# Kernel tuning notes

Measured on AMD Instinct MI355X. Metric: run time of the kernel, lower is better.

Reference implementation:

```python
import jax, jax.numpy as jnp
import numpy as np

BN_EPS = 1e-5

@jax.custom_vjp
def ste_sign(x):
    return jnp.sign(x)

def _ste_fwd(x):
    return jnp.sign(x), x

def _ste_bwd(x, g):
    # straight-through estimator with hardtanh clipping
    return (g * (jnp.abs(x) <= 1.0).astype(g.dtype),)

ste_sign.defvjp(_ste_fwd, _ste_bwd)

def bi_conv_bn_relu(h, W, scale, gamma, beta):
    # h: [B, Cin, K, N]; W: [Cout, Cin] (1x1 conv); scale/gamma/beta: [Cout]
    ba = ste_sign(h)                      # binarize activations
    bw = ste_sign(W)                      # binarize weights
    y = jnp.einsum('oi,bikn->bokn', bw, ba) * scale[None, :, None, None]
    # BatchNorm2d, training-mode batch statistics over (B, K, N)
    mean = jnp.mean(y, axis=(0, 2, 3), keepdims=True)
    var = jnp.var(y, axis=(0, 2, 3), keepdims=True)
    y = gamma[None, :, None, None] * (y - mean) * jax.lax.rsqrt(var + BN_EPS) + beta[None, :, None, None]
    return jax.nn.relu(y)

def setup_inputs() -> dict:
    key = jax.random.key(0)
    sizes = [64, 64, 64, 128]
    B, N, K = 8, 1024, 32
    ks = jax.random.split(key, 16)
    inp = {"agg_feat": jax.random.normal(ks[0], (B * N, K, sizes[0]), dtype=jnp.float32)}
    j = 1
    for i in range(1, len(sizes)):
        cin, cout = sizes[i - 1], sizes[i]
        inp[f"W{i}"] = jax.random.normal(ks[j], (cout, cin), dtype=jnp.float32) * 0.1; j += 1
        inp[f"s{i}"] = jax.random.uniform(ks[j], (cout,), dtype=jnp.float32, minval=0.05, maxval=0.2); j += 1
        inp[f"g{i}"] = jnp.ones((cout,), dtype=jnp.float32)
        inp[f"b{i}"] = jnp.zeros((cout,), dtype=jnp.float32)
    return inp

def reference(agg_feat, W1, s1, g1, b1, W2, s2, g2, b2, W3, s3, g3, b3):
    B = 8
    M, K, D = agg_feat.shape
    # view(B, -1, K, D).permute(0, 3, 2, 1) -> [B, D, K, N]
    h = agg_feat.reshape(B, M // B, K, D).transpose(0, 3, 2, 1)
    h = bi_conv_bn_relu(h, W1, s1, g1, b1)
    h = bi_conv_bn_relu(h, W2, s2, g2, b2)
    h = bi_conv_bn_relu(h, W3, s3, g3, b3)
    h = jnp.max(h, axis=2)                 # max-pool over neighbors -> [B, C, N]
    C = h.shape[1]
    return h.transpose(0, 2, 1).reshape(-1, C)  # [B*N, C]
```

## Files before the change

### kernel.cpp

```cpp
#include <hip/hip_runtime.h>


typedef unsigned long long u64;
typedef unsigned int u32;

#define P_TOTAL (8192 * 32)
#define NREP 16

__device__ __forceinline__ u64 bcast64(u64 x, int p) {
    unsigned lo = __builtin_amdgcn_readlane((unsigned)x, p);
    unsigned hi = __builtin_amdgcn_readlane((unsigned)(x >> 32), p);
    return ((u64)hi << 32) | lo;
}

__device__ __forceinline__ u64 pack_stats(int sd, int sq) {
    return ((u64)(unsigned)sd << 32) | (u64)(unsigned)sq;
}

__device__ __forceinline__ void affine_from_stats(const u64* __restrict__ st,
        int c, const float* __restrict__ scale, const float* __restrict__ gamma,
        const float* __restrict__ beta, int cparam, float& a, float& b) {
    u64 v = 0;
    #pragma unroll
    for (int r = 0; r < NREP; ++r) v += st[r * 256 + c];
    int sd = (int)(v >> 32);
    int sq = (int)(unsigned)(v & 0xFFFFFFFFull);
    const double invN = 1.0 / (double)P_TOTAL;
    double m = (double)sd * invN;
    double var = (double)sq * invN - m * m;
    double sc = (double)scale[cparam];
    double inv = 1.0 / sqrt(sc * sc * var + 1e-5);
    double g = (double)gamma[cparam];
    a = (float)(g * inv * sc);
    b = (float)((double)beta[cparam] - g * inv * sc * m);
}

__device__ __forceinline__ int make_thresh(float a, float b, bool& flip) {
    if (a == 0.f) { flip = false; return (b > 0.f) ? -65 : 65; }
    double r = -(double)b / (double)a;
    r = fmin(fmax(r, -1e6), 1e6);
    int t0 = (int)floor(r);
    int T;
    if (a > 0.f) {
        flip = false;
        T = t0 + 2;
        if (fmaf(a, (float)(t0 + 1), b) > 0.f) T = t0 + 1;
        if (fmaf(a, (float)(t0    ), b) > 0.f) T = t0;
        if (fmaf(a, (float)(t0 - 1), b) > 0.f) T = t0 - 1;
    } else {
        flip = true;
        int H = t0 - 2;
        if (fmaf(a, (float)(t0 - 1), b) > 0.f) H = t0 - 1;
        if (fmaf(a, (float)(t0    ), b) > 0.f) H = t0;
        if (fmaf(a, (float)(t0 + 1), b) > 0.f) H = t0 + 1;
        T = -H;
    }
    return max(-65, min(65, T));
}

__device__ __forceinline__ void block_params(const u64* __restrict__ stats,
        int stat_off, const float* __restrict__ scale, const float* __restrict__ gamma,
        const float* __restrict__ beta, int* gT, int* gF) {
    const int t = threadIdx.x;
    if (t < 64) {
        float a, b;
        affine_from_stats(stats, stat_off + t, scale, gamma, beta, t, a, b);
        bool flip;
        gT[t] = make_thresh(a, b, flip);
        gF[t] = flip ? 1 : 0;
    }
    __syncthreads();
}

__global__ void __launch_bounds__(256) k0_pack(
    const float* __restrict__ W1, const float* __restrict__ W2,
    const float* __restrict__ W3, ulonglong2* __restrict__ wp1,
    ulonglong2* __restrict__ wp2, ulonglong2* __restrict__ wp3,
    u64* __restrict__ stats) {
    const int t = threadIdx.x;
    #pragma unroll
    for (int r = 0; r < NREP; ++r) stats[r * 256 + t] = 0;

    const float* src;
    ulonglong2* dst;
    bool perm, l1;
    if (t < 64)       { src = W1 + t * 64;         dst = wp1 + t;         perm = true;  l1 = true;  }
    else if (t < 128) { src = W2 + (t - 64) * 64;  dst = wp2 + (t - 64);  perm = false; l1 = false; }
    else              { src = W3 + (t - 128) * 64; dst = wp3 + (t - 128); perm = false; l1 = false; }

    const float4* s4 = (const float4*)src;
    float4 v[16];
    #pragma unroll
    for (int j = 0; j < 16; ++j) v[j] = s4[j];

    u64 hiM = 0, loM = 0;
    #pragma unroll
    for (int j = 0; j < 16; ++j) {
        const float e0 = v[j].x, e1 = v[j].y, e2 = v[j].z, e3 = v[j].w;
        #pragma unroll
        for (int k = 0; k < 4; ++k) {
            const float w = (k == 0) ? e0 : (k == 1) ? e1 : (k == 2) ? e2 : e3;
            const int c = 4 * j + k;
            const int p = perm ? (((c & 3) << 4) | (c >> 2)) : c;
            const bool bh = (w > 0.f);
            const bool bl = l1 ? (w != 0.f) : (w < 0.f);
            if (bh) hiM |= 1ull << p;
            if (bl) loM |= 1ull << p;
        }
    }
    *dst = make_ulonglong2(hiM, loM);
}

__global__ void __launch_bounds__(256) k1_pack_stats(
    const float4* __restrict__ in4, const ulonglong2* __restrict__ wp1,
    ulonglong2* __restrict__ A1, u64* __restrict__ stats) {
    const int lane = threadIdx.x & 63;
    const int wib = threadIdx.x >> 6;
    const int wid = (blockIdx.x << 2) | wib;
    const ulonglong2 w = wp1[lane];
    const int sh = (lane >> 4) << 4;
    const size_t base = (size_t)wid * 512 + lane;

    float4 v0 = in4[base];
    float4 v1 = in4[base + 64];
    float4 v2 = in4[base + 128];
    float4 v3 = in4[base + 192];
    float4 v4 = in4[base + 256];
    float4 v5 = in4[base + 320];
    float4 v6 = in4[base + 384];
    float4 v7 = in4[base + 448];

    int sd = 0, sq = 0;
    auto proc = [&](float4 v, int q0) {
        u64 bs0 = __ballot(v.x > 0.f), bn0 = __ballot(v.x != 0.f);
        u64 bs1 = __ballot(v.y > 0.f), bn1 = __ballot(v.y != 0.f);
        u64 bs2 = __ballot(v.z > 0.f), bn2 = __ballot(v.z != 0.f);
        u64 bs3 = __ballot(v.w > 0.f), bn3 = __ballot(v.w != 0.f);
        u64 myS = ((bs0 >> sh) & 0xFFFFull) | (((bs1 >> sh) & 0xFFFFull) << 16)
                | (((bs2 >> sh) & 0xFFFFull) << 32) | (((bs3 >> sh) & 0xFFFFull) << 48);
        u64 myN = ((bn0 >> sh) & 0xFFFFull) | (((bn1 >> sh) & 0xFFFFull) << 16)
                | (((bn2 >> sh) & 0xFFFFull) << 32) | (((bn3 >> sh) & 0xFFFFull) << 48);
        if ((lane & 15) == 0) A1[q0 + (lane >> 4)] = make_ulonglong2(myS, myN);
        #pragma unroll
        for (int p = 0; p < 4; ++p) {
            const int s2 = p << 4;
            u64 as = ((bs0 >> s2) & 0xFFFFull) | (((bs1 >> s2) & 0xFFFFull) << 16)
                   | (((bs2 >> s2) & 0xFFFFull) << 32) | (((bs3 >> s2) & 0xFFFFull) << 48);
            u64 an = ((bn0 >> s2) & 0xFFFFull) | (((bn1 >> s2) & 0xFFFFull) << 16)
                   | (((bn2 >> s2) & 0xFFFFull) << 32) | (((bn3 >> s2) & 0xFFFFull) << 48);
            u64 mnz = an & w.y;
            int dot = __popcll(mnz) - 2 * __popcll(mnz & (as ^ w.x));
            sd += dot; sq += dot * dot;
        }
    };
    const int q_base = wid * 32;
    proc(v0, q_base);      proc(v1, q_base + 4);
    proc(v2, q_base + 8);  proc(v3, q_base + 12);
    proc(v4, q_base + 16); proc(v5, q_base + 20);
    proc(v6, q_base + 24); proc(v7, q_base + 28);

    __shared__ int rd[4][64], rq[4][64];
    rd[wib][lane] = sd; rq[wib][lane] = sq;
    __syncthreads();
    if (threadIdx.x < 64) {
        int td = rd[0][lane] + rd[1][lane] + rd[2][lane] + rd[3][lane];
        int tq = rq[0][lane] + rq[1][lane] + rq[2][lane] + rq[3][lane];
        atomicAdd(&stats[(blockIdx.x & (NREP - 1)) * 256 + lane], pack_stats(td, tq));
    }
}

__global__ void __launch_bounds__(256) k2_bin1_stats2(
    const ulonglong2* __restrict__ A1, const ulonglong2* __restrict__ wp1,
    const ulonglong2* __restrict__ wp2, const float* __restrict__ scale,
    const float* __restrict__ gamma, const float* __restrict__ beta,
    u64* __restrict__ A2, u64* __restrict__ stats) {
    __shared__ int gT[64], gF[64];
    block_params(stats, 0, scale, gamma, beta, gT, gF);

    const int lane = threadIdx.x & 63;
    const int wib = threadIdx.x >> 6;
    const int wid = (blockIdx.x << 2) | wib;
    const int T = gT[lane];
    const bool flip = gF[lane] != 0;
    ulonglong2 w1 = wp1[lane];
    const u64 w1S = flip ? ~w1.x : w1.x;
    const u64 w1N = w1.y;
    const ulonglong2 w2 = wp2[lane];

    const u64 av = ((const u64*)A1)[(size_t)wid * 64 + lane];
    u64 mymask = 0;
    int sd = 0, sq = 0;
    #pragma unroll 8
    for (int p = 0; p < 32; ++p) {
        u64 as = bcast64(av, 2 * p);
        u64 an = bcast64(av, 2 * p + 1);
        u64 mnz = an & w1N;
        int dot1 = __popcll(mnz) - 2 * __popcll(mnz & (as ^ w1S));
        u64 A = __ballot(dot1 >= T);
        if (lane == p) mymask = A;
        int d2 = __popcll(A & w2.x) - __popcll(A & w2.y);
        sd += d2; sq += d2 * d2;
    }
    if (lane < 32) A2[(size_t)wid * 32 + lane] = mymask;

    __shared__ int rd[4][64], rq[4][64];
    rd[wib][lane] = sd; rq[wib][lane] = sq;
    __syncthreads();
    if (threadIdx.x < 64) {
        int td = rd[0][lane] + rd[1][lane] + rd[2][lane] + rd[3][lane];
        int tq = rq[0][lane] + rq[1][lane] + rq[2][lane] + rq[3][lane];
        atomicAdd(&stats[(blockIdx.x & (NREP - 1)) * 256 + 64 + lane], pack_stats(td, tq));
    }
}

__global__ void __launch_bounds__(256) k3_bin2_stats3(
    const u64* __restrict__ A2, const ulonglong2* __restrict__ wp2,
    const ulonglong2* __restrict__ wp3, const float* __restrict__ scale,
    const float* __restrict__ gamma, const float* __restrict__ beta,
    short* __restrict__ dmm, u64* __restrict__ stats) {
    __shared__ int gT[64], gF[64];
    block_params(stats, 64, scale, gamma, beta, gT, gF);

    const int lane = threadIdx.x & 63;
    const int wib = threadIdx.x >> 6;
    const int wid = (blockIdx.x << 2) | wib;
    const int T = gT[lane];
    const bool flip = gF[lane] != 0;
    const ulonglong2 w2 = wp2[lane];
    const u64 w2P = flip ? w2.y : w2.x;
    const u64 w2N = flip ? w2.x : w2.y;
    const ulonglong2 w3a = wp3[lane];
    const ulonglong2 w3b = wp3[lane + 64];

    const u32 a32 = ((const u32*)A2)[(size_t)wid * 64 + lane];
    int sda = 0, sqa = 0, sdb = 0, sqb = 0;
    int maxa = -127, mina = 127, maxb = -127, minb = 127;
    #pragma unroll 8
    for (int p = 0; p < 32; ++p) {
        u32 lo = __builtin_amdgcn_readlane(a32, 2 * p);
        u32 hi = __builtin_amdgcn_readlane(a32, 2 * p + 1);
        u64 A = ((u64)hi << 32) | lo;
        int d2 = __popcll(A & w2P) - __popcll(A & w2N);
        u64 A3 = __ballot(d2 >= T);
        int da = __popcll(A3 & w3a.x) - __popcll(A3 & w3a.y);
        int db = __popcll(A3 & w3b.x) - __popcll(A3 & w3b.y);
        sda += da; sqa += da * da; sdb += db; sqb += db * db;
        maxa = max(maxa, da); mina = min(mina, da);
        maxb = max(maxb, db); minb = min(minb, db);
    }
    dmm[wid * 128 + lane]      = (short)((maxa & 0xFF) | ((mina & 0xFF) << 8));
    dmm[wid * 128 + 64 + lane] = (short)((maxb & 0xFF) | ((minb & 0xFF) << 8));

    __shared__ int rda[4][64], rqa[4][64], rdb[4][64], rqb[4][64];
    rda[wib][lane] = sda; rqa[wib][lane] = sqa;
    rdb[wib][lane] = sdb; rqb[wib][lane] = sqb;
    __syncthreads();
    if (threadIdx.x < 64) {
        const int rep = (blockIdx.x & (NREP - 1)) * 256;
        int tda = rda[0][lane] + rda[1][lane] + rda[2][lane] + rda[3][lane];
        int tqa = rqa[0][lane] + rqa[1][lane] + rqa[2][lane] + rqa[3][lane];
        int tdb = rdb[0][lane] + rdb[1][lane] + rdb[2][lane] + rdb[3][lane];
        int tqb = rqb[0][lane] + rqb[1][lane] + rqb[2][lane] + rqb[3][lane];
        atomicAdd(&stats[rep + 128 + lane], pack_stats(tda, tqa));
        atomicAdd(&stats[rep + 192 + lane], pack_stats(tdb, tqb));
    }
}

__global__ void __launch_bounds__(512) k4_out(
    const short* __restrict__ dmm, const float* __restrict__ scale,
    const float* __restrict__ gamma, const float* __restrict__ beta,
    const u64* __restrict__ stats, float* __restrict__ out) {
    __shared__ float sa[128], sb[128];
    if (threadIdx.x < 128)
        affine_from_stats(stats, 128 + threadIdx.x, scale, gamma, beta,
                          threadIdx.x, sa[threadIdx.x], sb[threadIdx.x]);
    __syncthreads();
    const int idx = blockIdx.x * 512 + threadIdx.x;
    const int o = idx & 127;
    short pk = dmm[idx];
    int mx = (signed char)(pk & 0xFF);
    int mn = (signed char)((pk >> 8) & 0xFF);
    float a = sa[o], b = sb[o];
    float v = fmaf(a, (float)(a >= 0.f ? mx : mn), b);
    out[idx] = fmaxf(v, 0.f);
}

extern "C" void kernel_launch(void* const* d_in, const int* in_sizes, int n_in,
                              void* d_out, int out_size, void* d_ws, size_t ws_size,
                              hipStream_t stream) {
    const float* agg = (const float*)d_in[0];
    const float* W1 = (const float*)d_in[1];
    const float* s1 = (const float*)d_in[2];
    const float* g1 = (const float*)d_in[3];
    const float* b1 = (const float*)d_in[4];
    const float* W2 = (const float*)d_in[5];
    const float* s2 = (const float*)d_in[6];
    const float* g2 = (const float*)d_in[7];
    const float* b2 = (const float*)d_in[8];
    const float* W3 = (const float*)d_in[9];
    const float* s3 = (const float*)d_in[10];
    const float* g3 = (const float*)d_in[11];
    const float* b3 = (const float*)d_in[12];
    float* out = (float*)d_out;

    char* ws = (char*)d_ws;
    ulonglong2* wp1 = (ulonglong2*)(ws + 0);
    ulonglong2* wp2 = (ulonglong2*)(ws + 1024);
    ulonglong2* wp3 = (ulonglong2*)(ws + 2048);
    u64* stats = (u64*)(ws + 4096);
    ulonglong2* A1 = (ulonglong2*)(ws + 65536);
    u64* A2 = (u64*)(ws + 65536 + (size_t)P_TOTAL * 16);
    short* dmm = (short*)(ws + 65536 + (size_t)P_TOTAL * 24);

    k0_pack<<<1, 256, 0, stream>>>(W1, W2, W3, wp1, wp2, wp3, stats);
    k1_pack_stats<<<2048, 256, 0, stream>>>((const float4*)agg, wp1, A1, stats);
    k2_bin1_stats2<<<2048, 256, 0, stream>>>(A1, wp1, wp2, s1, g1, b1, A2, stats);
    k3_bin2_stats3<<<2048, 256, 0, stream>>>(A2, wp2, wp3, s2, g2, b2, dmm, stats);
    k4_out<<<2048, 512, 0, stream>>>(dmm, s3, g3, b3, stats, out);
}
```

Before: 72.18 us.

## Fuse all stages into one persistent kernel with grid-wide barriers

Replaces the five-kernel pipeline with a stats-zeroing kernel and a single persistent kernel of 512 blocks. Each wave keeps its binarized intermediate masks in registers across the three layers and synchronizes via atomic grid barriers between the batch-norm statistics phases. This removes the global-memory round trips for the A1/A2/dmm intermediates and the extra kernel launches. In exchange it relies on all 512 blocks being co-resident (launch bounds 256,2) and adds spin-wait barrier latency.

```diff
diff --git a/kernel.cpp b/kernel.cpp
--- a/kernel.cpp
+++ b/kernel.cpp
@@ -6,6 +6,7 @@
 
 #define P_TOTAL (8192 * 32)
 #define NREP 16
+#define NBLK 512
 
 __device__ __forceinline__ u64 bcast64(u64 x, int p) {
     unsigned lo = __builtin_amdgcn_readlane((unsigned)x, p);
@@ -17,12 +18,17 @@
     return ((u64)(unsigned)sd << 32) | (u64)(unsigned)sq;
 }
 
-__device__ __forceinline__ void affine_from_stats(const u64* __restrict__ st,
-        int c, const float* __restrict__ scale, const float* __restrict__ gamma,
+__device__ __forceinline__ void stat_add(u64* p, u64 v) {
+    __hip_atomic_fetch_add(p, v, __ATOMIC_RELEASE, __HIP_MEMORY_SCOPE_AGENT);
+}
+
+__device__ __forceinline__ void affine_from_stats(u64* st, int c,
+        const float* __restrict__ scale, const float* __restrict__ gamma,
         const float* __restrict__ beta, int cparam, float& a, float& b) {
     u64 v = 0;
     #pragma unroll
-    for (int r = 0; r < NREP; ++r) v += st[r * 256 + c];
+    for (int r = 0; r < NREP; ++r)
+        v += __hip_atomic_load(&st[r * 256 + c], __ATOMIC_RELAXED, __HIP_MEMORY_SCOPE_AGENT);
     int sd = (int)(v >> 32);
     int sq = (int)(unsigned)(v & 0xFFFFFFFFull);
     const double invN = 1.0 / (double)P_TOTAL;
@@ -58,237 +64,226 @@
     return max(-65, min(65, T));
 }
 
-__device__ __forceinline__ void block_params(const u64* __restrict__ stats,
-        int stat_off, const float* __restrict__ scale, const float* __restrict__ gamma,
-        const float* __restrict__ beta, int* gT, int* gF) {
-    const int t = threadIdx.x;
-    if (t < 64) {
-        float a, b;
-        affine_from_stats(stats, stat_off + t, scale, gamma, beta, t, a, b);
-        bool flip;
-        gT[t] = make_thresh(a, b, flip);
-        gF[t] = flip ? 1 : 0;
-    }
-    __syncthreads();
-}
-
-__global__ void __launch_bounds__(256) k0_pack(
-    const float* __restrict__ W1, const float* __restrict__ W2,
-    const float* __restrict__ W3, ulonglong2* __restrict__ wp1,
-    ulonglong2* __restrict__ wp2, ulonglong2* __restrict__ wp3,
-    u64* __restrict__ stats) {
-    const int t = threadIdx.x;
-    #pragma unroll
-    for (int r = 0; r < NREP; ++r) stats[r * 256 + t] = 0;
-
-    const float* src;
-    ulonglong2* dst;
-    bool perm, l1;
-    if (t < 64)       { src = W1 + t * 64;         dst = wp1 + t;         perm = true;  l1 = true;  }
-    else if (t < 128) { src = W2 + (t - 64) * 64;  dst = wp2 + (t - 64);  perm = false; l1 = false; }
-    else              { src = W3 + (t - 128) * 64; dst = wp3 + (t - 128); perm = false; l1 = false; }
-
-    const float4* s4 = (const float4*)src;
-    float4 v[16];
-    #pragma unroll
-    for (int j = 0; j < 16; ++j) v[j] = s4[j];
-
-    u64 hiM = 0, loM = 0;
-    #pragma unroll
-    for (int j = 0; j < 16; ++j) {
-        const float e0 = v[j].x, e1 = v[j].y, e2 = v[j].z, e3 = v[j].w;
-        #pragma unroll
-        for (int k = 0; k < 4; ++k) {
-            const float w = (k == 0) ? e0 : (k == 1) ? e1 : (k == 2) ? e2 : e3;
-            const int c = 4 * j + k;
-            const int p = perm ? (((c & 3) << 4) | (c >> 2)) : c;
-            const bool bh = (w > 0.f);
-            const bool bl = l1 ? (w != 0.f) : (w < 0.f);
-            if (bh) hiM |= 1ull << p;
-            if (bl) loM |= 1ull << p;
-        }
-    }
-    *dst = make_ulonglong2(hiM, loM);
-}
-
-__global__ void __launch_bounds__(256) k1_pack_stats(
-    const float4* __restrict__ in4, const ulonglong2* __restrict__ wp1,
-    ulonglong2* __restrict__ A1, u64* __restrict__ stats) {
+__device__ __forceinline__ void gbar(u32* bar, int k) {
+    __syncthreads();
+    if (threadIdx.x == 0) {
+        __hip_atomic_fetch_add(&bar[k], 1u, __ATOMIC_ACQ_REL, __HIP_MEMORY_SCOPE_AGENT);
+        while (__hip_atomic_load(&bar[k], __ATOMIC_ACQUIRE, __HIP_MEMORY_SCOPE_AGENT) < (u32)NBLK)
+            __builtin_amdgcn_s_sleep(2);
+    }
+    __syncthreads();
+}
+
+__global__ void k_zero(u64* __restrict__ stats, u32* __restrict__ bar) {
+    stats[blockIdx.x * 256 + threadIdx.x] = 0;
+    if (blockIdx.x == 0 && threadIdx.x < 16) bar[threadIdx.x] = 0;
+}
+
+__global__ void __launch_bounds__(256, 2) kmain(
+    const float4* __restrict__ in4,
+    const float* __restrict__ W1, const float* __restrict__ s1,
+    const float* __restrict__ g1, const float* __restrict__ b1,
+    const float* __restrict__ W2, const float* __restrict__ s2,
+    const float* __restrict__ g2, const float* __restrict__ b2,
+    const float* __restrict__ W3, const float* __restrict__ s3,
+    const float* __restrict__ g3, const float* __restrict__ b3,
+    float* __restrict__ out, u64* __restrict__ stats, u32* __restrict__ bar) {
     const int lane = threadIdx.x & 63;
     const int wib = threadIdx.x >> 6;
-    const int wid = (blockIdx.x << 2) | wib;
-    const ulonglong2 w = wp1[lane];
-    const int sh = (lane >> 4) << 4;
-    const size_t base = (size_t)wid * 512 + lane;
-
-    float4 v0 = in4[base];
-    float4 v1 = in4[base + 64];
-    float4 v2 = in4[base + 128];
-    float4 v3 = in4[base + 192];
-    float4 v4 = in4[base + 256];
-    float4 v5 = in4[base + 320];
-    float4 v6 = in4[base + 384];
-    float4 v7 = in4[base + 448];
-
-    int sd = 0, sq = 0;
-    auto proc = [&](float4 v, int q0) {
-        u64 bs0 = __ballot(v.x > 0.f), bn0 = __ballot(v.x != 0.f);
-        u64 bs1 = __ballot(v.y > 0.f), bn1 = __ballot(v.y != 0.f);
-        u64 bs2 = __ballot(v.z > 0.f), bn2 = __ballot(v.z != 0.f);
-        u64 bs3 = __ballot(v.w > 0.f), bn3 = __ballot(v.w != 0.f);
-        u64 myS = ((bs0 >> sh) & 0xFFFFull) | (((bs1 >> sh) & 0xFFFFull) << 16)
-                | (((bs2 >> sh) & 0xFFFFull) << 32) | (((bs3 >> sh) & 0xFFFFull) << 48);
-        u64 myN = ((bn0 >> sh) & 0xFFFFull) | (((bn1 >> sh) & 0xFFFFull) << 16)
-                | (((bn2 >> sh) & 0xFFFFull) << 32) | (((bn3 >> sh) & 0xFFFFull) << 48);
-        if ((lane & 15) == 0) A1[q0 + (lane >> 4)] = make_ulonglong2(myS, myN);
-        #pragma unroll
-        for (int p = 0; p < 4; ++p) {
-            const int s2 = p << 4;
-            u64 as = ((bs0 >> s2) & 0xFFFFull) | (((bs1 >> s2) & 0xFFFFull) << 16)
-                   | (((bs2 >> s2) & 0xFFFFull) << 32) | (((bs3 >> s2) & 0xFFFFull) << 48);
-            u64 an = ((bn0 >> s2) & 0xFFFFull) | (((bn1 >> s2) & 0xFFFFull) << 16)
-                   | (((bn2 >> s2) & 0xFFFFull) << 32) | (((bn3 >> s2) & 0xFFFFull) << 48);
-            u64 mnz = an & w.y;
-            int dot = __popcll(mnz) - 2 * __popcll(mnz & (as ^ w.x));
-            sd += dot; sq += dot * dot;
-        }
-    };
-    const int q_base = wid * 32;
-    proc(v0, q_base);      proc(v1, q_base + 4);
-    proc(v2, q_base + 8);  proc(v3, q_base + 12);
-    proc(v4, q_base + 16); proc(v5, q_base + 20);
-    proc(v6, q_base + 24); proc(v7, q_base + 28);
-
-    __shared__ int rd[4][64], rq[4][64];
-    rd[wib][lane] = sd; rq[wib][lane] = sq;
-    __syncthreads();
+    const int gw = blockIdx.x * 4 + wib;
+    const int rep = (blockIdx.x & (NREP - 1)) * 256;
+
+    __shared__ int rda[4][64], rqa[4][64], rdb[4][64], rqb[4][64];
+    __shared__ int gT[64], gF[64];
+    __shared__ float sA[128], sB[128];
+
+    u64 w1S = 0, w1N = 0, w2P = 0, w2N = 0, w3aP = 0, w3aN = 0, w3bP = 0, w3bN = 0;
+    {
+        const float4* r1 = (const float4*)(W1 + lane * 64);
+        const float4* r2 = (const float4*)(W2 + lane * 64);
+        const float4* r3a = (const float4*)(W3 + lane * 64);
+        const float4* r3b = (const float4*)(W3 + (lane + 64) * 64);
+        #pragma unroll
+        for (int j = 0; j < 16; ++j) {
+            float4 a = r1[j], b = r2[j], c = r3a[j], d = r3b[j];
+            #pragma unroll
+            for (int k = 0; k < 4; ++k) {
+                const int ch = 4 * j + k;
+                const int p1 = ((ch & 3) << 4) | (ch >> 2);
+                float wa = (k == 0) ? a.x : (k == 1) ? a.y : (k == 2) ? a.z : a.w;
+                float wb = (k == 0) ? b.x : (k == 1) ? b.y : (k == 2) ? b.z : b.w;
+                float wc = (k == 0) ? c.x : (k == 1) ? c.y : (k == 2) ? c.z : c.w;
+                float wd = (k == 0) ? d.x : (k == 1) ? d.y : (k == 2) ? d.z : d.w;
+                if (wa > 0.f)  w1S |= 1ull << p1;
+                if (wa != 0.f) w1N |= 1ull << p1;
+                if (wb > 0.f)  w2P |= 1ull << ch;
+                if (wb < 0.f)  w2N |= 1ull << ch;
+                if (wc > 0.f)  w3aP |= 1ull << ch;
+                if (wc < 0.f)  w3aN |= 1ull << ch;
+                if (wd > 0.f)  w3bP |= 1ull << ch;
+                if (wd < 0.f)  w3bN |= 1ull << ch;
+            }
+        }
+    }
+
+    u64 a1s[4], a1n[4];
+    {
+        int sd = 0, sq = 0;
+        #pragma unroll
+        for (int un = 0; un < 4; ++un) {
+            const size_t base = (size_t)(4 * gw + un) * 512 + lane;
+            float4 v0 = in4[base];
+            float4 v1 = in4[base + 64];
+            float4 v2 = in4[base + 128];
+            float4 v3 = in4[base + 192];
+            float4 v4 = in4[base + 256];
+            float4 v5 = in4[base + 320];
+            float4 v6 = in4[base + 384];
+            float4 v7 = in4[base + 448];
+            u64 ms = 0, mn = 0;
+            auto proc = [&](float4 v, int b) {
+                u64 bs0 = __ballot(v.x > 0.f), bn0 = __ballot(v.x != 0.f);
+                u64 bs1 = __ballot(v.y > 0.f), bn1 = __ballot(v.y != 0.f);
+                u64 bs2 = __ballot(v.z > 0.f), bn2 = __ballot(v.z != 0.f);
+                u64 bs3 = __ballot(v.w > 0.f), bn3 = __ballot(v.w != 0.f);
+                #pragma unroll
+                for (int p = 0; p < 4; ++p) {
+                    const int s2 = p << 4;
+                    u64 as = ((bs0 >> s2) & 0xFFFFull) | (((bs1 >> s2) & 0xFFFFull) << 16)
+                           | (((bs2 >> s2) & 0xFFFFull) << 32) | (((bs3 >> s2) & 0xFFFFull) << 48);
+                    u64 an = ((bn0 >> s2) & 0xFFFFull) | (((bn1 >> s2) & 0xFFFFull) << 16)
+                           | (((bn2 >> s2) & 0xFFFFull) << 32) | (((bn3 >> s2) & 0xFFFFull) << 48);
+                    u64 mnz = an & w1N;
+                    int dot = __popcll(mnz) - 2 * __popcll(mnz & (as ^ w1S));
+                    sd += dot; sq += dot * dot;
+                    if (lane == b * 4 + p) { ms = as; mn = an; }
+                }
+            };
+            proc(v0, 0); proc(v1, 1); proc(v2, 2); proc(v3, 3);
+            proc(v4, 4); proc(v5, 5); proc(v6, 6); proc(v7, 7);
+            a1s[un] = ms; a1n[un] = mn;
+        }
+        rda[wib][lane] = sd; rqa[wib][lane] = sq;
+        __syncthreads();
+        if (threadIdx.x < 64) {
+            int td = rda[0][lane] + rda[1][lane] + rda[2][lane] + rda[3][lane];
+            int tq = rqa[0][lane] + rqa[1][lane] + rqa[2][lane] + rqa[3][lane];
+            stat_add(&stats[rep + lane], pack_stats(td, tq));
+            __threadfence();
+        }
+    }
+    gbar(bar, 0);
+
     if (threadIdx.x < 64) {
-        int td = rd[0][lane] + rd[1][lane] + rd[2][lane] + rd[3][lane];
-        int tq = rq[0][lane] + rq[1][lane] + rq[2][lane] + rq[3][lane];
-        atomicAdd(&stats[(blockIdx.x & (NREP - 1)) * 256 + lane], pack_stats(td, tq));
-    }
-}
-
-__global__ void __launch_bounds__(256) k2_bin1_stats2(
-    const ulonglong2* __restrict__ A1, const ulonglong2* __restrict__ wp1,
-    const ulonglong2* __restrict__ wp2, const float* __restrict__ scale,
-    const float* __restrict__ gamma, const float* __restrict__ beta,
-    u64* __restrict__ A2, u64* __restrict__ stats) {
-    __shared__ int gT[64], gF[64];
-    block_params(stats, 0, scale, gamma, beta, gT, gF);
-
-    const int lane = threadIdx.x & 63;
-    const int wib = threadIdx.x >> 6;
-    const int wid = (blockIdx.x << 2) | wib;
-    const int T = gT[lane];
-    const bool flip = gF[lane] != 0;
-    ulonglong2 w1 = wp1[lane];
-    const u64 w1S = flip ? ~w1.x : w1.x;
-    const u64 w1N = w1.y;
-    const ulonglong2 w2 = wp2[lane];
-
-    const u64 av = ((const u64*)A1)[(size_t)wid * 64 + lane];
-    u64 mymask = 0;
-    int sd = 0, sq = 0;
-    #pragma unroll 8
-    for (int p = 0; p < 32; ++p) {
-        u64 as = bcast64(av, 2 * p);
-        u64 an = bcast64(av, 2 * p + 1);
-        u64 mnz = an & w1N;
-        int dot1 = __popcll(mnz) - 2 * __popcll(mnz & (as ^ w1S));
-        u64 A = __ballot(dot1 >= T);
-        if (lane == p) mymask = A;
-        int d2 = __popcll(A & w2.x) - __popcll(A & w2.y);
-        sd += d2; sq += d2 * d2;
-    }
-    if (lane < 32) A2[(size_t)wid * 32 + lane] = mymask;
-
-    __shared__ int rd[4][64], rq[4][64];
-    rd[wib][lane] = sd; rq[wib][lane] = sq;
-    __syncthreads();
+        float a, b;
+        affine_from_stats(stats, threadIdx.x, s1, g1, b1, threadIdx.x, a, b);
+        bool fl;
+        gT[threadIdx.x] = make_thresh(a, b, fl);
+        gF[threadIdx.x] = fl ? 1 : 0;
+    }
+    __syncthreads();
+    u64 a2m[4];
+    {
+        const int T = gT[lane];
+        const u64 w1Sf = gF[lane] ? ~w1S : w1S;
+        int sd = 0, sq = 0;
+        #pragma unroll
+        for (int un = 0; un < 4; ++un) {
+            u64 mymask = 0;
+            #pragma unroll 8
+            for (int p = 0; p < 32; ++p) {
+                u64 as = bcast64(a1s[un], p);
+                u64 an = bcast64(a1n[un], p);
+                u64 mnz = an & w1N;
+                int dot1 = __popcll(mnz) - 2 * __popcll(mnz & (as ^ w1Sf));
+                u64 A = __ballot(dot1 >= T);
+                if (lane == p) mymask = A;
+                int d2 = __popcll(A & w2P) - __popcll(A & w2N);
+                sd += d2; sq += d2 * d2;
+            }
+            a2m[un] = mymask;
+        }
+        __syncthreads();
+        rda[wib][lane] = sd; rqa[wib][lane] = sq;
+        __syncthreads();
+        if (threadIdx.x < 64) {
+            int td = rda[0][lane] + rda[1][lane] + rda[2][lane] + rda[3][lane];
+            int tq = rqa[0][lane] + rqa[1][lane] + rqa[2][lane] + rqa[3][lane];
+            stat_add(&stats[rep + 64 + lane], pack_stats(td, tq));
+            __threadfence();
+        }
+    }
+    gbar(bar, 1);
+
     if (threadIdx.x < 64) {
-        int td = rd[0][lane] + rd[1][lane] + rd[2][lane] + rd[3][lane];
-        int tq = rq[0][lane] + rq[1][lane] + rq[2][lane] + rq[3][lane];
-        atomicAdd(&stats[(blockIdx.x & (NREP - 1)) * 256 + 64 + lane], pack_stats(td, tq));
-    }
-}
-
-__global__ void __launch_bounds__(256) k3_bin2_stats3(
-    const u64* __restrict__ A2, const ulonglong2* __restrict__ wp2,
-    const ulonglong2* __restrict__ wp3, const float* __restrict__ scale,
-    const float* __restrict__ gamma, const float* __restrict__ beta,
-    short* __restrict__ dmm, u64* __restrict__ stats) {
-    __shared__ int gT[64], gF[64];
-    block_params(stats, 64, scale, gamma, beta, gT, gF);
-
-    const int lane = threadIdx.x & 63;
-    const int wib = threadIdx.x >> 6;
-    const int wid = (blockIdx.x << 2) | wib;
-    const int T = gT[lane];
-    const bool flip = gF[lane] != 0;
-    const ulonglong2 w2 = wp2[lane];
-    const u64 w2P = flip ? w2.y : w2.x;
-    const u64 w2N = flip ? w2.x : w2.y;
-    const ulonglong2 w3a = wp3[lane];
-    const ulonglong2 w3b = wp3[lane + 64];
-
-    const u32 a32 = ((const u32*)A2)[(size_t)wid * 64 + lane];
-    int sda = 0, sqa = 0, sdb = 0, sqb = 0;
-    int maxa = -127, mina = 127, maxb = -127, minb = 127;
-    #pragma unroll 8
-    for (int p = 0; p < 32; ++p) {
-        u32 lo = __builtin_amdgcn_readlane(a32, 2 * p);
-        u32 hi = __builtin_amdgcn_readlane(a32, 2 * p + 1);
-        u64 A = ((u64)hi << 32) | lo;
-        int d2 = __popcll(A & w2P) - __popcll(A & w2N);
-        u64 A3 = __ballot(d2 >= T);
-        int da = __popcll(A3 & w3a.x) - __popcll(A3 & w3a.y);
-        int db = __popcll(A3 & w3b.x) - __popcll(A3 & w3b.y);
-        sda += da; sqa += da * da; sdb += db; sqb += db * db;
-        maxa = max(maxa, da); mina = min(mina, da);
-        maxb = max(maxb, db); minb = min(minb, db);
-    }
-    dmm[wid * 128 + lane]      = (short)((maxa & 0xFF) | ((mina & 0xFF) << 8));
-    dmm[wid * 128 + 64 + lane] = (short)((maxb & 0xFF) | ((minb & 0xFF) << 8));
-
-    __shared__ int rda[4][64], rqa[4][64], rdb[4][64], rqb[4][64];
-    rda[wib][lane] = sda; rqa[wib][lane] = sqa;
-    rdb[wib][lane] = sdb; rqb[wib][lane] = sqb;
-    __syncthreads();
-    if (threadIdx.x < 64) {
-        const int rep = (blockIdx.x & (NREP - 1)) * 256;
-        int tda = rda[0][lane] + rda[1][lane] + rda[2][lane] + rda[3][lane];
-        int tqa = rqa[0][lane] + rqa[1][lane] + rqa[2][lane] + rqa[3][lane];
-        int tdb = rdb[0][lane] + rdb[1][lane] + rdb[2][lane] + rdb[3][lane];
-        int tqb = rqb[0][lane] + rqb[1][lane] + rqb[2][lane] + rqb[3][lane];
-        atomicAdd(&stats[rep + 128 + lane], pack_stats(tda, tqa));
-        atomicAdd(&stats[rep + 192 + lane], pack_stats(tdb, tqb));
-    }
-}
-
-__global__ void __launch_bounds__(512) k4_out(
-    const short* __restrict__ dmm, const float* __restrict__ scale,
-    const float* __restrict__ gamma, const float* __restrict__ beta,
-    const u64* __restrict__ stats, float* __restrict__ out) {
-    __shared__ float sa[128], sb[128];
-    if (threadIdx.x < 128)
-        affine_from_stats(stats, 128 + threadIdx.x, scale, gamma, beta,
-                          threadIdx.x, sa[threadIdx.x], sb[threadIdx.x]);
-    __syncthreads();
-    const int idx = blockIdx.x * 512 + threadIdx.x;
-    const int o = idx & 127;
-    short pk = dmm[idx];
-    int mx = (signed char)(pk & 0xFF);
-    int mn = (signed char)((pk >> 8) & 0xFF);
-    float a = sa[o], b = sb[o];
-    float v = fmaf(a, (float)(a >= 0.f ? mx : mn), b);
-    out[idx] = fmaxf(v, 0.f);
+        float a, b;
+        affine_from_stats(stats, 64 + threadIdx.x, s2, g2, b2, threadIdx.x, a, b);
+        bool fl;
+        gT[threadIdx.x] = make_thresh(a, b, fl);
+        gF[threadIdx.x] = fl ? 1 : 0;
+    }
+    __syncthreads();
+    int mxa[4], mna[4], mxb[4], mnb[4];
+    {
+        const int T = gT[lane];
+        const u64 w2Pf = gF[lane] ? w2N : w2P;
+        const u64 w2Nf = gF[lane] ? w2P : w2N;
+        int sda = 0, sqa = 0, sdb = 0, sqb = 0;
+        #pragma unroll
+        for (int un = 0; un < 4; ++un) {
+            int xa = -127, na = 127, xb = -127, nb = 127;
+            #pragma unroll 8
+            for (int p = 0; p < 32; ++p) {
+                u64 A = bcast64(a2m[un], p);
+                int d2 = __popcll(A & w2Pf) - __popcll(A & w2Nf);
+                u64 A3 = __ballot(d2 >= T);
+                int da = __popcll(A3 & w3aP) - __popcll(A3 & w3aN);
+                int db = __popcll(A3 & w3bP) - __popcll(A3 & w3bN);
+                sda += da; sqa += da * da; sdb += db; sqb += db * db;
+                xa = max(xa, da); na = min(na, da);
+                xb = max(xb, db); nb = min(nb, db);
+            }
+            mxa[un] = xa; mna[un] = na; mxb[un] = xb; mnb[un] = nb;
+        }
+        __syncthreads();
+        rda[wib][lane] = sda; rqa[wib][lane] = sqa;
+        rdb[wib][lane] = sdb; rqb[wib][lane] = sqb;
+        __syncthreads();
+        if (threadIdx.x < 64) {
+            int tda = rda[0][lane] + rda[1][lane] + rda[2][lane] + rda[3][lane];
+            int tqa = rqa[0][lane] + rqa[1][lane] + rqa[2][lane] + rqa[3][lane];
+            int tdb = rdb[0][lane] + rdb[1][lane] + rdb[2][lane] + rdb[3][lane];
+            int tqb = rqb[0][lane] + rqb[1][lane] + rqb[2][lane] + rqb[3][lane];
+            stat_add(&stats[rep + 128 + lane], pack_stats(tda, tqa));
+            stat_add(&stats[rep + 192 + lane], pack_stats(tdb, tqb));
+            __threadfence();
+        }
+    }
+    gbar(bar, 2);
+
+    if (threadIdx.x < 128) {
+        affine_from_stats(stats, 128 + threadIdx.x, s3, g3, b3, threadIdx.x,
+                          sA[threadIdx.x], sB[threadIdx.x]);
+    }
+    __syncthreads();
+    {
+        const float aa = sA[lane], ba = sB[lane];
+        const float ab = sA[64 + lane], bb = sB[64 + lane];
+        #pragma unroll
+        for (int un = 0; un < 4; ++un) {
+            const int m = 4 * gw + un;
+            float va = fmaf(aa, (float)(aa >= 0.f ? mxa[un] : mna[un]), ba);
+            float vb = fmaf(ab, (float)(ab >= 0.f ? mxb[un] : mnb[un]), bb);
+            out[(size_t)m * 128 + lane] = fmaxf(va, 0.f);
+            out[(size_t)m * 128 + 64 + lane] = fmaxf(vb, 0.f);
+        }
+    }
 }
 
 extern "C" void kernel_launch(void* const* d_in, const int* in_sizes, int n_in,
                               void* d_out, int out_size, void* d_ws, size_t ws_size,
                               hipStream_t stream) {
-    const float* agg = (const float*)d_in[0];
+    const float4* in4 = (const float4*)d_in[0];
     const float* W1 = (const float*)d_in[1];
     const float* s1 = (const float*)d_in[2];
     const float* g1 = (const float*)d_in[3];
@@ -302,19 +297,10 @@
     const float* g3 = (const float*)d_in[11];
     const float* b3 = (const float*)d_in[12];
     float* out = (float*)d_out;
-
-    char* ws = (char*)d_ws;
-    ulonglong2* wp1 = (ulonglong2*)(ws + 0);
-    ulonglong2* wp2 = (ulonglong2*)(ws + 1024);
-    ulonglong2* wp3 = (ulonglong2*)(ws + 2048);
-    u64* stats = (u64*)(ws + 4096);
-    ulonglong2* A1 = (ulonglong2*)(ws + 65536);
-    u64* A2 = (u64*)(ws + 65536 + (size_t)P_TOTAL * 16);
-    short* dmm = (short*)(ws + 65536 + (size_t)P_TOTAL * 24);
-
-    k0_pack<<<1, 256, 0, stream>>>(W1, W2, W3, wp1, wp2, wp3, stats);
-    k1_pack_stats<<<2048, 256, 0, stream>>>((const float4*)agg, wp1, A1, stats);
-    k2_bin1_stats2<<<2048, 256, 0, stream>>>(A1, wp1, wp2, s1, g1, b1, A2, stats);
-    k3_bin2_stats3<<<2048, 256, 0, stream>>>(A2, wp2, wp3, s2, g2, b2, dmm, stats);
-    k4_out<<<2048, 512, 0, stream>>>(dmm, s3, g3, b3, stats, out);
-}
+    u64* stats = (u64*)d_ws;
+    u32* bar = (u32*)((char*)d_ws + 32768);
+
+    k_zero<<<16, 256, 0, stream>>>(stats, bar);
+    kmain<<<NBLK, 256, 0, stream>>>(in4, W1, s1, g1, b1, W2, s2, g2, b2,
+                                    W3, s3, g3, b3, out, stats, bar);
+}
```

New measurement: 220.8 us. 3.06x slower.

## Fold weight packing into each kernel and replace pack kernel with memset

Applied to the files above, without the earlier changes.

Removes the single-block weight-packing kernel. Each consumer kernel now packs the binarized weight rows it needs into shared memory, and the stats buffer is cleared with an async memset. The BN threshold computation runs in parallel with the weight packing on separate thread groups. The inner loops of k2 and k3 are fully unrolled with two independent accumulator sets to shorten the dependency chains. In exchange, every block repeats the weight loads and packing, which adds redundant global reads and prologue latency per block.

```diff
diff --git a/kernel.cpp b/kernel.cpp
--- a/kernel.cpp
+++ b/kernel.cpp
@@ -58,66 +58,42 @@
     return max(-65, min(65, T));
 }
 
-__device__ __forceinline__ void block_params(const u64* __restrict__ stats,
-        int stat_off, const float* __restrict__ scale, const float* __restrict__ gamma,
-        const float* __restrict__ beta, int* gT, int* gF) {
-    const int t = threadIdx.x;
-    if (t < 64) {
-        float a, b;
-        affine_from_stats(stats, stat_off + t, scale, gamma, beta, t, a, b);
-        bool flip;
-        gT[t] = make_thresh(a, b, flip);
-        gF[t] = flip ? 1 : 0;
-    }
-    __syncthreads();
-}
-
-__global__ void __launch_bounds__(256) k0_pack(
-    const float* __restrict__ W1, const float* __restrict__ W2,
-    const float* __restrict__ W3, ulonglong2* __restrict__ wp1,
-    ulonglong2* __restrict__ wp2, ulonglong2* __restrict__ wp3,
-    u64* __restrict__ stats) {
-    const int t = threadIdx.x;
-    #pragma unroll
-    for (int r = 0; r < NREP; ++r) stats[r * 256 + t] = 0;
-
-    const float* src;
-    ulonglong2* dst;
-    bool perm, l1;
-    if (t < 64)       { src = W1 + t * 64;         dst = wp1 + t;         perm = true;  l1 = true;  }
-    else if (t < 128) { src = W2 + (t - 64) * 64;  dst = wp2 + (t - 64);  perm = false; l1 = false; }
-    else              { src = W3 + (t - 128) * 64; dst = wp3 + (t - 128); perm = false; l1 = false; }
-
+__device__ __forceinline__ void pack_row(const float* __restrict__ src, bool perm,
+                                         bool l1m, u64& hiM, u64& loM) {
     const float4* s4 = (const float4*)src;
-    float4 v[16];
-    #pragma unroll
-    for (int j = 0; j < 16; ++j) v[j] = s4[j];
-
-    u64 hiM = 0, loM = 0;
+    hiM = 0; loM = 0;
     #pragma unroll
     for (int j = 0; j < 16; ++j) {
-        const float e0 = v[j].x, e1 = v[j].y, e2 = v[j].z, e3 = v[j].w;
+        float4 v = s4[j];
         #pragma unroll
         for (int k = 0; k < 4; ++k) {
-            const float w = (k == 0) ? e0 : (k == 1) ? e1 : (k == 2) ? e2 : e3;
+            const float w = (k == 0) ? v.x : (k == 1) ? v.y : (k == 2) ? v.z : v.w;
             const int c = 4 * j + k;
             const int p = perm ? (((c & 3) << 4) | (c >> 2)) : c;
             const bool bh = (w > 0.f);
-            const bool bl = l1 ? (w != 0.f) : (w < 0.f);
+            const bool bl = l1m ? (w != 0.f) : (w < 0.f);
             if (bh) hiM |= 1ull << p;
             if (bl) loM |= 1ull << p;
         }
     }
-    *dst = make_ulonglong2(hiM, loM);
 }
 
 __global__ void __launch_bounds__(256) k1_pack_stats(
-    const float4* __restrict__ in4, const ulonglong2* __restrict__ wp1,
+    const float4* __restrict__ in4, const float* __restrict__ W1,
     ulonglong2* __restrict__ A1, u64* __restrict__ stats) {
+    __shared__ u64 wl[128];
+    if (threadIdx.x < 64) {
+        u64 h, l;
+        pack_row(W1 + threadIdx.x * 64, true, true, h, l);
+        wl[2 * threadIdx.x] = h;
+        wl[2 * threadIdx.x + 1] = l;
+    }
+    __syncthreads();
+
     const int lane = threadIdx.x & 63;
     const int wib = threadIdx.x >> 6;
     const int wid = (blockIdx.x << 2) | wib;
-    const ulonglong2 w = wp1[lane];
+    const u64 w1S = wl[2 * lane], w1N = wl[2 * lane + 1];
     const int sh = (lane >> 4) << 4;
     const size_t base = (size_t)wid * 512 + lane;
 
@@ -148,8 +124,8 @@
                    | (((bs2 >> s2) & 0xFFFFull) << 32) | (((bs3 >> s2) & 0xFFFFull) << 48);
             u64 an = ((bn0 >> s2) & 0xFFFFull) | (((bn1 >> s2) & 0xFFFFull) << 16)
                    | (((bn2 >> s2) & 0xFFFFull) << 32) | (((bn3 >> s2) & 0xFFFFull) << 48);
-            u64 mnz = an & w.y;
-            int dot = __popcll(mnz) - 2 * __popcll(mnz & (as ^ w.x));
+            u64 mnz = an & w1N;
+            int dot = __popcll(mnz) - 2 * __popcll(mnz & (as ^ w1S));
             sd += dot; sq += dot * dot;
         }
     };
@@ -170,41 +146,73 @@
 }
 
 __global__ void __launch_bounds__(256) k2_bin1_stats2(
-    const ulonglong2* __restrict__ A1, const ulonglong2* __restrict__ wp1,
-    const ulonglong2* __restrict__ wp2, const float* __restrict__ scale,
+    const ulonglong2* __restrict__ A1, const float* __restrict__ W1,
+    const float* __restrict__ W2, const float* __restrict__ scale,
     const float* __restrict__ gamma, const float* __restrict__ beta,
     u64* __restrict__ A2, u64* __restrict__ stats) {
+    __shared__ u64 wl[256];
     __shared__ int gT[64], gF[64];
-    block_params(stats, 0, scale, gamma, beta, gT, gF);
+    {
+        const int t = threadIdx.x;
+        if (t < 64) {
+            u64 h, l;
+            pack_row(W1 + t * 64, true, true, h, l);
+            wl[2 * t] = h; wl[2 * t + 1] = l;
+        } else if (t < 128) {
+            u64 h, l;
+            pack_row(W2 + (t - 64) * 64, false, false, h, l);
+            wl[2 * t] = h; wl[2 * t + 1] = l;
+        } else if (t < 192) {
+            const int c = t - 128;
+            float a, b;
+            affine_from_stats(stats, c, scale, gamma, beta, c, a, b);
+            bool fl;
+            gT[c] = make_thresh(a, b, fl);
+            gF[c] = fl ? 1 : 0;
+        }
+    }
+    __syncthreads();
 
     const int lane = threadIdx.x & 63;
     const int wib = threadIdx.x >> 6;
     const int wid = (blockIdx.x << 2) | wib;
     const int T = gT[lane];
-    const bool flip = gF[lane] != 0;
-    ulonglong2 w1 = wp1[lane];
-    const u64 w1S = flip ? ~w1.x : w1.x;
-    const u64 w1N = w1.y;
-    const ulonglong2 w2 = wp2[lane];
+    const u64 w1S = gF[lane] ? ~wl[2 * lane] : wl[2 * lane];
+    const u64 w1N = wl[2 * lane + 1];
+    const u64 w2P = wl[128 + 2 * lane], w2N = wl[129 + 2 * lane];
 
     const u64 av = ((const u64*)A1)[(size_t)wid * 64 + lane];
     u64 mymask = 0;
-    int sd = 0, sq = 0;
-    #pragma unroll 8
-    for (int p = 0; p < 32; ++p) {
-        u64 as = bcast64(av, 2 * p);
-        u64 an = bcast64(av, 2 * p + 1);
-        u64 mnz = an & w1N;
-        int dot1 = __popcll(mnz) - 2 * __popcll(mnz & (as ^ w1S));
-        u64 A = __ballot(dot1 >= T);
-        if (lane == p) mymask = A;
-        int d2 = __popcll(A & w2.x) - __popcll(A & w2.y);
-        sd += d2; sq += d2 * d2;
+    int sd0 = 0, sq0 = 0, sd1 = 0, sq1 = 0;
+    #pragma unroll
+    for (int pp = 0; pp < 16; ++pp) {
+        {
+            const int p = 2 * pp;
+            u64 as = bcast64(av, 2 * p);
+            u64 an = bcast64(av, 2 * p + 1);
+            u64 mnz = an & w1N;
+            int dot1 = __popcll(mnz) - 2 * __popcll(mnz & (as ^ w1S));
+            u64 A = __ballot(dot1 >= T);
+            if (lane == p) mymask = A;
+            int d2 = __popcll(A & w2P) - __popcll(A & w2N);
+            sd0 += d2; sq0 += d2 * d2;
+        }
+        {
+            const int p = 2 * pp + 1;
+            u64 as = bcast64(av, 2 * p);
+            u64 an = bcast64(av, 2 * p + 1);
+            u64 mnz = an & w1N;
+            int dot1 = __popcll(mnz) - 2 * __popcll(mnz & (as ^ w1S));
+            u64 A = __ballot(dot1 >= T);
+            if (lane == p) mymask = A;
+            int d2 = __popcll(A & w2P) - __popcll(A & w2N);
+            sd1 += d2; sq1 += d2 * d2;
+        }
     }
     if (lane < 32) A2[(size_t)wid * 32 + lane] = mymask;
 
     __shared__ int rd[4][64], rq[4][64];
-    rd[wib][lane] = sd; rq[wib][lane] = sq;
+    rd[wib][lane] = sd0 + sd1; rq[wib][lane] = sq0 + sq1;
     __syncthreads();
     if (threadIdx.x < 64) {
         int td = rd[0][lane] + rd[1][lane] + rd[2][lane] + rd[3][lane];
@@ -214,46 +222,82 @@
 }
 
 __global__ void __launch_bounds__(256) k3_bin2_stats3(
-    const u64* __restrict__ A2, const ulonglong2* __restrict__ wp2,
-    const ulonglong2* __restrict__ wp3, const float* __restrict__ scale,
+    const u64* __restrict__ A2, const float* __restrict__ W2,
+    const float* __restrict__ W3, const float* __restrict__ scale,
     const float* __restrict__ gamma, const float* __restrict__ beta,
     short* __restrict__ dmm, u64* __restrict__ stats) {
+    __shared__ u64 wl[384];
     __shared__ int gT[64], gF[64];
-    block_params(stats, 64, scale, gamma, beta, gT, gF);
+    {
+        const int t = threadIdx.x;
+        if (t < 64) {
+            u64 h, l;
+            pack_row(W2 + t * 64, false, false, h, l);
+            wl[2 * t] = h; wl[2 * t + 1] = l;
+        } else if (t < 192) {
+            const int r = t - 64;
+            u64 h, l;
+            pack_row(W3 + r * 64, false, false, h, l);
+            wl[128 + 2 * r] = h; wl[129 + 2 * r] = l;
+        } else {
+            const int c = t - 192;
+            float a, b;
+            affine_from_stats(stats, 64 + c, scale, gamma, beta, c, a, b);
+            bool fl;
+            gT[c] = make_thresh(a, b, fl);
+            gF[c] = fl ? 1 : 0;
+        }
+    }
+    __syncthreads();
 
     const int lane = threadIdx.x & 63;
     const int wib = threadIdx.x >> 6;
     const int wid = (blockIdx.x << 2) | wib;
     const int T = gT[lane];
-    const bool flip = gF[lane] != 0;
-    const ulonglong2 w2 = wp2[lane];
-    const u64 w2P = flip ? w2.y : w2.x;
-    const u64 w2N = flip ? w2.x : w2.y;
-    const ulonglong2 w3a = wp3[lane];
-    const ulonglong2 w3b = wp3[lane + 64];
+    const u64 w2P = gF[lane] ? wl[2 * lane + 1] : wl[2 * lane];
+    const u64 w2N = gF[lane] ? wl[2 * lane] : wl[2 * lane + 1];
+    const u64 w3aP = wl[128 + 2 * lane], w3aN = wl[129 + 2 * lane];
+    const u64 w3bP = wl[128 + 2 * (lane + 64)], w3bN = wl[129 + 2 * (lane + 64)];
 
     const u32 a32 = ((const u32*)A2)[(size_t)wid * 64 + lane];
-    int sda = 0, sqa = 0, sdb = 0, sqb = 0;
+    int sda0 = 0, sqa0 = 0, sdb0 = 0, sqb0 = 0;
+    int sda1 = 0, sqa1 = 0, sdb1 = 0, sqb1 = 0;
     int maxa = -127, mina = 127, maxb = -127, minb = 127;
-    #pragma unroll 8
-    for (int p = 0; p < 32; ++p) {
-        u32 lo = __builtin_amdgcn_readlane(a32, 2 * p);
-        u32 hi = __builtin_amdgcn_readlane(a32, 2 * p + 1);
-        u64 A = ((u64)hi << 32) | lo;
-        int d2 = __popcll(A & w2P) - __popcll(A & w2N);
-        u64 A3 = __ballot(d2 >= T);
-        int da = __popcll(A3 & w3a.x) - __popcll(A3 & w3a.y);
-        int db = __popcll(A3 & w3b.x) - __popcll(A3 & w3b.y);
-        sda += da; sqa += da * da; sdb += db; sqb += db * db;
-        maxa = max(maxa, da); mina = min(mina, da);
-        maxb = max(maxb, db); minb = min(minb, db);
+    #pragma unroll
+    for (int pp = 0; pp < 16; ++pp) {
+        {
+            const int p = 2 * pp;
+            u32 lo = __builtin_amdgcn_readlane(a32, 2 * p);
+            u32 hi = __builtin_amdgcn_readlane(a32, 2 * p + 1);
+            u64 A = ((u64)hi << 32) | lo;
+            int d2 = __popcll(A & w2P) - __popcll(A & w2N);
+            u64 A3 = __ballot(d2 >= T);
+            int da = __popcll(A3 & w3aP) - __popcll(A3 & w3aN);
+            int db = __popcll(A3 & w3bP) - __popcll(A3 & w3bN);
+            sda0 += da; sqa0 += da * da; sdb0 += db; sqb0 += db * db;
+            maxa = max(maxa, da); mina = min(mina, da);
+            maxb = max(maxb, db); minb = min(minb, db);
+        }
+        {
+            const int p = 2 * pp + 1;
+            u32 lo = __builtin_amdgcn_readlane(a32, 2 * p);
+            u32 hi = __builtin_amdgcn_readlane(a32, 2 * p + 1);
+            u64 A = ((u64)hi << 32) | lo;
+            int d2 = __popcll(A & w2P) - __popcll(A & w2N);
+            u64 A3 = __ballot(d2 >= T);
+            int da = __popcll(A3 & w3aP) - __popcll(A3 & w3aN);
+            int db = __popcll(A3 & w3bP) - __popcll(A3 & w3bN);
+            sda1 += da; sqa1 += da * da; sdb1 += db; sqb1 += db * db;
+            maxa = max(maxa, da); mina = min(mina, da);
+            maxb = max(maxb, db); minb = min(minb, db);
+        }
     }
     dmm[wid * 128 + lane]      = (short)((maxa & 0xFF) | ((mina & 0xFF) << 8));
     dmm[wid * 128 + 64 + lane] = (short)((maxb & 0xFF) | ((minb & 0xFF) << 8));
 
     __shared__ int rda[4][64], rqa[4][64], rdb[4][64], rqb[4][64];
-    rda[wib][lane] = sda; rqa[wib][lane] = sqa;
-    rdb[wib][lane] = sdb; rqb[wib][lane] = sqb;
+    rda[wib][lane] = sda0 + sda1; rqa[wib][lane] = sqa0 + sqa1;
+    rdb[wib][lane] = sdb0 + sdb1; rqb[wib][lane] = sqb0 + sqb1;
     __syncthreads();
     if (threadIdx.x < 64) {
         const int rep = (blockIdx.x & (NREP - 1)) * 256;
@@ -304,17 +348,14 @@
     float* out = (float*)d_out;
 
     char* ws = (char*)d_ws;
-    ulonglong2* wp1 = (ulonglong2*)(ws + 0);
-    ulonglong2* wp2 = (ulonglong2*)(ws + 1024);
-    ulonglong2* wp3 = (ulonglong2*)(ws + 2048);
-    u64* stats = (u64*)(ws + 4096);
+    u64* stats = (u64*)ws;
     ulonglong2* A1 = (ulonglong2*)(ws + 65536);
     u64* A2 = (u64*)(ws + 65536 + (size_t)P_TOTAL * 16);
     short* dmm = (short*)(ws + 65536 + (size_t)P_TOTAL * 24);
 
-    k0_pack<<<1, 256, 0, stream>>>(W1, W2, W3, wp1, wp2, wp3, stats);
-    k1_pack_stats<<<2048, 256, 0, stream>>>((const float4*)agg, wp1, A1, stats);
-    k2_bin1_stats2<<<2048, 256, 0, stream>>>(A1, wp1, wp2, s1, g1, b1, A2, stats);
-    k3_bin2_stats3<<<2048, 256, 0, stream>>>(A2, wp2, wp3, s2, g2, b2, dmm, stats);
+    hipMemsetAsync(stats, 0, NREP * 256 * sizeof(u64), stream);
+    k1_pack_stats<<<2048, 256, 0, stream>>>((const float4*)agg, W1, A1, stats);
+    k2_bin1_stats2<<<2048, 256, 0, stream>>>(A1, W1, W2, s1, g1, b1, A2, stats);
+    k3_bin2_stats3<<<2048, 256, 0, stream>>>(A2, W2, W3, s2, g2, b2, dmm, stats);
     k4_out<<<2048, 512, 0, stream>>>(dmm, s3, g3, b3, stats, out);
 }
```

New measurement: 83.40 us. +15.6%, slower.
